# Kernel optimization log

Hardware: AMD Instinct MI355X
Metric: run time of the kernel (lower is better)

## Reference

```python
import jax, jax.numpy as jnp
import numpy as np

N_NODES = 50000
D_FEAT = 128
N_EDGES_1 = 800_000
N_EDGES_2 = 2_400_000


def setup_inputs() -> dict:
    key = jax.random.key(0)
    k = jax.random.split(key, 7)
    x = jax.random.normal(k[0], (N_NODES, D_FEAT), dtype=jnp.float32)
    row1 = jax.random.randint(k[1], (N_EDGES_1,), 0, N_NODES, dtype=jnp.int32)
    col1 = jax.random.randint(k[2], (N_EDGES_1,), 0, N_NODES, dtype=jnp.int32)
    vals1 = jax.random.uniform(k[3], (N_EDGES_1,), dtype=jnp.float32)
    row2 = jax.random.randint(k[4], (N_EDGES_2,), 0, N_NODES, dtype=jnp.int32)
    col2 = jax.random.randint(k[5], (N_EDGES_2,), 0, N_NODES, dtype=jnp.int32)
    vals2 = jax.random.uniform(k[6], (N_EDGES_2,), dtype=jnp.float32)
    return {"x": x, "row1": row1, "col1": col1, "vals1": vals1,
            "row2": row2, "col2": col2, "vals2": vals2}


def _spmm(row, col, vals, x, n_nodes):
    # (A @ x)[i] = sum_{e: row[e]==i} vals[e] * x[col[e]]
    msgs = vals[:, None] * x[col]          # [E, d] gathered, weighted messages
    return jax.ops.segment_sum(msgs, row, num_segments=n_nodes)  # [N, d]


def reference(x, row1, col1, vals1, row2, col2, vals2):
    x1 = _spmm(row1, col1, vals1, x, N_NODES)   # 1-hop aggregation
    x2 = _spmm(row2, col2, vals2, x, N_NODES)   # 2-hop aggregation
    return jnp.concatenate([x1, x2], axis=1)    # [N, 2d]
```

## Files before the change

kernel.cpp:

```cpp
#include <hip/hip_runtime.h>


constexpr int D = 128;
constexpr int OUT_STRIDE = 256;
constexpr int NBMAX = 800;
constexpr int BATCH = 8192;
constexpr int LRECS = 3840;

struct KP {
  const float* x;
  const int* row1; const int* col1; const float* vals1;
  const int* row2; const int* col2; const float* vals2;
  float* out;
  int n, e1, e2, nx4, nb, cap1, cap2, t1, ntasks;
  int* gcur;
  unsigned short* xb;
  uint2* seg1;
  uint2* seg2;
};

__device__ __forceinline__ unsigned short f2b(float f) {
  unsigned u = __float_as_uint(f);
  u += 0x7fffu + ((u >> 16) & 1u);
  return (unsigned short)(u >> 16);
}
__device__ __forceinline__ float blo(unsigned u) { return __uint_as_float(u << 16); }
__device__ __forceinline__ float bhi(unsigned u) { return __uint_as_float(u & 0xffff0000u); }

__global__ void zero_k(KP p) {
  for (int j = threadIdx.x; j < 2 * p.nb; j += 256) p.gcur[j] = 0;
}

__launch_bounds__(512, 2)
__global__ void scatter_k(KP p) {
  __shared__ uint2 srecs[BATCH];
  __shared__ int cnts[NBMAX];
  __shared__ int lstart[NBMAX];
  __shared__ int wsum[8];
  const int tid  = threadIdx.x;
  const int lane = tid & 63;
  const int wid  = tid >> 6;
  const int nb   = p.nb;

  const int task  = blockIdx.x;
  const int hop   = (task >= p.t1);
  const int tbase = (hop ? (task - p.t1) : task) * BATCH;
  const int E     = hop ? p.e2 : p.e1;
  const int m     = min(BATCH, E - tbase);
  const int* rowp = hop ? p.row2 : p.row1;
  const int* colp = hop ? p.col2 : p.col1;
  const float* vp = hop ? p.vals2 : p.vals1;
  const int cap   = hop ? p.cap2 : p.cap1;
  uint2* seg      = hop ? p.seg2 : p.seg1;
  int* gc         = p.gcur + (hop ? nb : 0);

  {
    const int per  = (p.nx4 + (int)gridDim.x - 1) / (int)gridDim.x;
    const int jend = min(p.nx4, (task + 1) * per);
    for (int j = task * per + tid; j < jend; j += 512) {
      const float4 v = ((const float4*)p.x)[j];
      ushort4 o; o.x = f2b(v.x); o.y = f2b(v.y); o.z = f2b(v.z); o.w = f2b(v.w);
      ((ushort4*)p.xb)[j] = o;
    }
  }

  for (int b = tid; b < NBMAX; b += 512) cnts[b] = 0;

  int   rowv[16]; int colv[16]; float valv[16];
  #pragma unroll
  for (int k = 0; k < 4; ++k) {
    const int i4 = tid + (k << 9);
    const int e0 = i4 << 2;
    if (e0 + 3 < m) {
      const int4  r = ((const int4*)(rowp + tbase))[i4];
      const int4  c = ((const int4*)(colp + tbase))[i4];
      const float4 v = ((const float4*)(vp + tbase))[i4];
      rowv[k*4+0] = r.x; rowv[k*4+1] = r.y; rowv[k*4+2] = r.z; rowv[k*4+3] = r.w;
      colv[k*4+0] = c.x; colv[k*4+1] = c.y; colv[k*4+2] = c.z; colv[k*4+3] = c.w;
      valv[k*4+0] = v.x; valv[k*4+1] = v.y; valv[k*4+2] = v.z; valv[k*4+3] = v.w;
    } else {
      #pragma unroll
      for (int c2 = 0; c2 < 4; ++c2) {
        const int e = e0 + c2;
        if (e < m) {
          rowv[k*4+c2] = rowp[tbase + e];
          colv[k*4+c2] = colp[tbase + e];
          valv[k*4+c2] = vp[tbase + e];
        } else {
          rowv[k*4+c2] = -1; colv[k*4+c2] = 0; valv[k*4+c2] = 0.f;
        }
      }
    }
  }
  __syncthreads();

  #pragma unroll
  for (int i = 0; i < 16; ++i) {
    const int r = rowv[i];
    if (r >= 0) {
      const int rk = atomicAdd(&cnts[r >> 6], 1);
      rowv[i] = r | (rk << 16);
    }
  }
  __syncthreads();

  int c0 = 0, c1 = 0, s = 0;
  const int b0 = tid * 2;
  if (b0 < NBMAX) {
    c0 = cnts[b0]; c1 = cnts[b0 + 1];
    s = c0 + c1;
  }
  int acc = s;
  #pragma unroll
  for (int d = 1; d < 64; d <<= 1) { int t = __shfl_up(acc, d); if (lane >= d) acc += t; }
  if (lane == 63) wsum[wid] = acc;
  __syncthreads();
  int woff = 0;
  #pragma unroll
  for (int w = 0; w < 8; ++w) if (w < wid) woff += wsum[w];
  if (b0 < NBMAX) {
    const int ex = woff + acc - s;
    lstart[b0]     = ex;
    lstart[b0 + 1] = ex + c0;
  }
  __syncthreads();

  for (int i = tid; i < nb; i += 512) {
    const int b = (i + task * 37) % nb;
    const int c = cnts[b];
    if (c) {
      const int g = atomicAdd(&gc[b], c);
      cnts[b] = g - lstart[b];
    }
  }
  __syncthreads();

  #pragma unroll
  for (int i = 0; i < 16; ++i) {
    const int rv = rowv[i];
    if (rv >= 0) {
      const int r  = rv & 0xFFFF;
      const int rk = rv >> 16;
      const int b  = r >> 6;
      const unsigned meta = (unsigned)colv[i] | ((unsigned)(r & 63) << 16) | ((unsigned)b << 22);
      srecs[lstart[b] + rk] = make_uint2(meta, __float_as_uint(valv[i]));
    }
  }
  __syncthreads();

  for (int t = tid; t < m; t += 512) {
    const uint2 rec = srecs[t];
    const int b = rec.x >> 22;
    const int pos = t + cnts[b];
    if (pos < cap) seg[(size_t)b * cap + pos] = rec;
  }
}

__launch_bounds__(256)
__global__ void sort_gather_k(KP p) {
  __shared__ uint2 lrecs[LRECS];
  __shared__ int rstart[65];
  __shared__ int lcur[64];
  const int tid  = threadIdx.x;
  const int lane = tid & 63;
  const int wid  = tid >> 6;
  const int nb   = p.nb;
  const int hop  = (blockIdx.x < nb) ? 1 : 0;
  const int b    = hop ? blockIdx.x : blockIdx.x - nb;
  const int cap  = hop ? p.cap2 : p.cap1;
  const uint2* seg = (hop ? p.seg2 : p.seg1) + (size_t)b * cap;
  const int cnt  = min(p.gcur[(hop ? nb : 0) + b], cap);
  const uint4* xq = (const uint4*)p.xb;

  if (tid < 64) lcur[tid] = 0;
  __syncthreads();
  for (int t = tid; t < cnt; t += 256)
    atomicAdd(&lcur[(seg[t].x >> 16) & 63u], 1);
  __syncthreads();

  if (tid < 64) {
    const int c = lcur[tid];
    int acc = c;
    #pragma unroll
    for (int d = 1; d < 64; d <<= 1) { int t = __shfl_up(acc, d); if (lane >= d) acc += t; }
    const int ex = acc - c;
    rstart[tid] = ex;
    lcur[tid] = ex;
    if (tid == 63) rstart[64] = acc;
  }
  __syncthreads();

  for (int t = tid; t < cnt; t += 256) {
    const uint2 rec = seg[t];
    const int rl = (int)((rec.x >> 16) & 63u);
    const int pos = atomicAdd(&lcur[rl], 1);
    lrecs[pos] = rec;
  }
  __syncthreads();

  const int g   = lane >> 4;
  const int sub = lane & 15;
  const int rbase = b * 64;

  for (int r = wid; r < 64; r += 4) {
    const int rg = rbase + r;
    if (rg >= p.n) break;
    const int rs = rstart[r];
    const int re = rstart[r + 1];
    float a0 = 0.f, a1 = 0.f, a2 = 0.f, a3 = 0.f;
    float a4 = 0.f, a5 = 0.f, a6 = 0.f, a7 = 0.f;
    if (re > rs) {
      auto LD = [&](int idx, float& v, uint4& xv) {
        const uint2 q = lrecs[idx < re ? idx : re - 1];
        v = (idx < re) ? __uint_as_float(q.y) : 0.f;
        xv = xq[(q.x & 0xffffu) * 16u + (unsigned)sub];
      };
      #define FMA_G(v, xv)                                            \
        a0 = fmaf(v, blo(xv.x), a0); a1 = fmaf(v, bhi(xv.x), a1);     \
        a2 = fmaf(v, blo(xv.y), a2); a3 = fmaf(v, bhi(xv.y), a3);     \
        a4 = fmaf(v, blo(xv.z), a4); a5 = fmaf(v, bhi(xv.z), a5);     \
        a6 = fmaf(v, blo(xv.w), a6); a7 = fmaf(v, bhi(xv.w), a7);

      float v0, v1, v2, v3; uint4 x0, x1, x2, x3;
      const int j0 = rs + g;
      LD(j0, v0, x0); LD(j0 + 4, v1, x1); LD(j0 + 8, v2, x2); LD(j0 + 12, v3, x3);
      const int iters = (re - rs + 15) >> 4;
      for (int it = 1; it < iters; ++it) {
        const int jn = j0 + (it << 4);
        FMA_G(v0, x0); LD(jn,      v0, x0);
        FMA_G(v1, x1); LD(jn + 4,  v1, x1);
        FMA_G(v2, x2); LD(jn + 8,  v2, x2);
        FMA_G(v3, x3); LD(jn + 12, v3, x3);
      }
      FMA_G(v0, x0); FMA_G(v1, x1); FMA_G(v2, x2); FMA_G(v3, x3);
      #undef FMA_G

      a0 += __shfl_xor(a0, 16); a0 += __shfl_xor(a0, 32);
      a1 += __shfl_xor(a1, 16); a1 += __shfl_xor(a1, 32);
      a2 += __shfl_xor(a2, 16); a2 += __shfl_xor(a2, 32);
      a3 += __shfl_xor(a3, 16); a3 += __shfl_xor(a3, 32);
      a4 += __shfl_xor(a4, 16); a4 += __shfl_xor(a4, 32);
      a5 += __shfl_xor(a5, 16); a5 += __shfl_xor(a5, 32);
      a6 += __shfl_xor(a6, 16); a6 += __shfl_xor(a6, 32);
      a7 += __shfl_xor(a7, 16); a7 += __shfl_xor(a7, 32);
    }
    if (g == 0) {
      float* op = p.out + (size_t)rg * OUT_STRIDE + hop * D + sub * 8;
      ((float4*)op)[0] = make_float4(a0, a1, a2, a3);
      ((float4*)op)[1] = make_float4(a4, a5, a6, a7);
    }
  }
}

extern "C" void kernel_launch(void* const* d_in, const int* in_sizes, int n_in,
                              void* d_out, int out_size, void* d_ws, size_t ws_size,
                              hipStream_t stream) {
  KP p;
  p.x     = (const float*)d_in[0];
  p.row1  = (const int*)  d_in[1];
  p.col1  = (const int*)  d_in[2];
  p.vals1 = (const float*)d_in[3];
  p.row2  = (const int*)  d_in[4];
  p.col2  = (const int*)  d_in[5];
  p.vals2 = (const float*)d_in[6];
  p.out   = (float*)d_out;

  p.e1  = in_sizes[1];
  p.e2  = in_sizes[4];
  p.n   = out_size / OUT_STRIDE;
  p.nx4 = in_sizes[0] / 4;
  p.nb  = (p.n + 63) >> 6;
  if (p.nb > NBMAX || p.n > 65535) return;

  {
    const float m1 = (float)p.e1 / p.nb, m2 = (float)p.e2 / p.nb;
    p.cap1 = ((int)(m1 + 10.f * __builtin_sqrtf(m1) + 64.f) + 7) & ~7;
    p.cap2 = ((int)(m2 + 10.f * __builtin_sqrtf(m2) + 64.f) + 7) & ~7;
    if (p.cap1 > LRECS) p.cap1 = LRECS;
    if (p.cap2 > LRECS) p.cap2 = LRECS;
  }
  p.t1     = (p.e1 + BATCH - 1) / BATCH;
  p.ntasks = p.t1 + (p.e2 + BATCH - 1) / BATCH;

  char* w = (char*)d_ws;
  size_t off = 0;
  p.gcur = (int*)w;                       off += (size_t)(2 * p.nb) * 4;
  off = (off + 15) & ~(size_t)15;
  p.xb   = (unsigned short*)(w + off);    off += (size_t)in_sizes[0] * 2;
  off = (off + 15) & ~(size_t)15;
  p.seg1 = (uint2*)(w + off);             off += (size_t)p.nb * p.cap1 * 8;
  p.seg2 = (uint2*)(w + off);             off += (size_t)p.nb * p.cap2 * 8;
  if (ws_size < off) return;

  zero_k       <<<1,        256, 0, stream>>>(p);
  scatter_k    <<<p.ntasks, 512, 0, stream>>>(p);
  sort_gather_k<<<2 * p.nb, 256, 0, stream>>>(p);
}
```

Baseline: 252.7 us.

## Split sort and gather, quarter-feature bf16 layout for cache-local gathers

Stores the bf16 copy of x split into four 32-feature quarters, each laid out contiguously across nodes. The old sort+gather kernel is split into a sort kernel, which writes the row-sorted records back to the segment buffer along with row offsets, and a gather kernel. In the gather kernel each block handles a single feature quarter, so the working set of x it touches is a quarter of the size and should fit better in L2/MALL. The cost is an extra kernel launch, an extra write and read of the sorted records, and re-reading the records once per quarter.

```diff
diff --git a/kernel.cpp b/kernel.cpp
--- a/kernel.cpp
+++ b/kernel.cpp
@@ -12,8 +12,9 @@
   const int* row1; const int* col1; const float* vals1;
   const int* row2; const int* col2; const float* vals2;
   float* out;
-  int n, e1, e2, nx4, nb, cap1, cap2, t1, ntasks;
+  int n, e1, e2, nx4, nb, cap1, cap2, t1, ntasks, gq;
   int* gcur;
+  int* rstart_g;
   unsigned short* xb;
   uint2* seg1;
   uint2* seg2;
@@ -60,7 +61,11 @@
     for (int j = task * per + tid; j < jend; j += 512) {
       const float4 v = ((const float4*)p.x)[j];
       ushort4 o; o.x = f2b(v.x); o.y = f2b(v.y); o.z = f2b(v.z); o.w = f2b(v.w);
-      ((ushort4*)p.xb)[j] = o;
+      const int node = j >> 5;
+      const int f4   = j & 31;
+      const int q    = f4 >> 3;
+      const int k    = f4 & 7;
+      ((ushort4*)p.xb)[((size_t)q * p.n + node) * 8 + k] = o;
     }
   }
 
@@ -106,10 +111,7 @@
 
   int c0 = 0, c1 = 0, s = 0;
   const int b0 = tid * 2;
-  if (b0 < NBMAX) {
-    c0 = cnts[b0]; c1 = cnts[b0 + 1];
-    s = c0 + c1;
-  }
+  if (b0 < NBMAX) { c0 = cnts[b0]; c1 = cnts[b0 + 1]; s = c0 + c1; }
   int acc = s;
   #pragma unroll
   for (int d = 1; d < 64; d <<= 1) { int t = __shfl_up(acc, d); if (lane >= d) acc += t; }
@@ -157,25 +159,28 @@
 }
 
 __launch_bounds__(256)
-__global__ void sort_gather_k(KP p) {
+__global__ void sortseg_k(KP p) {
   __shared__ uint2 lrecs[LRECS];
-  __shared__ int rstart[65];
   __shared__ int lcur[64];
+  __shared__ int rst[65];
   const int tid  = threadIdx.x;
   const int lane = tid & 63;
-  const int wid  = tid >> 6;
   const int nb   = p.nb;
   const int hop  = (blockIdx.x < nb) ? 1 : 0;
   const int b    = hop ? blockIdx.x : blockIdx.x - nb;
   const int cap  = hop ? p.cap2 : p.cap1;
-  const uint2* seg = (hop ? p.seg2 : p.seg1) + (size_t)b * cap;
+  uint2* seg     = (hop ? p.seg2 : p.seg1) + (size_t)b * cap;
   const int cnt  = min(p.gcur[(hop ? nb : 0) + b], cap);
-  const uint4* xq = (const uint4*)p.xb;
-
+  const int pair = (int)blockIdx.x;
+
+  uint2 rr[15];
   if (tid < 64) lcur[tid] = 0;
   __syncthreads();
-  for (int t = tid; t < cnt; t += 256)
-    atomicAdd(&lcur[(seg[t].x >> 16) & 63u], 1);
+  #pragma unroll
+  for (int k = 0; k < 15; ++k) {
+    const int t = tid + (k << 8);
+    if (t < cnt) { rr[k] = seg[t]; atomicAdd(&lcur[(rr[k].x >> 16) & 63u], 1); }
+  }
   __syncthreads();
 
   if (tid < 64) {
@@ -184,71 +189,92 @@
     #pragma unroll
     for (int d = 1; d < 64; d <<= 1) { int t = __shfl_up(acc, d); if (lane >= d) acc += t; }
     const int ex = acc - c;
-    rstart[tid] = ex;
+    rst[tid] = ex;
     lcur[tid] = ex;
-    if (tid == 63) rstart[64] = acc;
-  }
-  __syncthreads();
-
-  for (int t = tid; t < cnt; t += 256) {
-    const uint2 rec = seg[t];
-    const int rl = (int)((rec.x >> 16) & 63u);
-    const int pos = atomicAdd(&lcur[rl], 1);
-    lrecs[pos] = rec;
-  }
-  __syncthreads();
-
-  const int g   = lane >> 4;
-  const int sub = lane & 15;
-  const int rbase = b * 64;
-
-  for (int r = wid; r < 64; r += 4) {
-    const int rg = rbase + r;
-    if (rg >= p.n) break;
-    const int rs = rstart[r];
-    const int re = rstart[r + 1];
-    float a0 = 0.f, a1 = 0.f, a2 = 0.f, a3 = 0.f;
-    float a4 = 0.f, a5 = 0.f, a6 = 0.f, a7 = 0.f;
-    if (re > rs) {
-      auto LD = [&](int idx, float& v, uint4& xv) {
-        const uint2 q = lrecs[idx < re ? idx : re - 1];
-        v = (idx < re) ? __uint_as_float(q.y) : 0.f;
-        xv = xq[(q.x & 0xffffu) * 16u + (unsigned)sub];
-      };
-      #define FMA_G(v, xv)                                            \
-        a0 = fmaf(v, blo(xv.x), a0); a1 = fmaf(v, bhi(xv.x), a1);     \
-        a2 = fmaf(v, blo(xv.y), a2); a3 = fmaf(v, bhi(xv.y), a3);     \
-        a4 = fmaf(v, blo(xv.z), a4); a5 = fmaf(v, bhi(xv.z), a5);     \
-        a6 = fmaf(v, blo(xv.w), a6); a7 = fmaf(v, bhi(xv.w), a7);
-
-      float v0, v1, v2, v3; uint4 x0, x1, x2, x3;
-      const int j0 = rs + g;
-      LD(j0, v0, x0); LD(j0 + 4, v1, x1); LD(j0 + 8, v2, x2); LD(j0 + 12, v3, x3);
-      const int iters = (re - rs + 15) >> 4;
-      for (int it = 1; it < iters; ++it) {
-        const int jn = j0 + (it << 4);
-        FMA_G(v0, x0); LD(jn,      v0, x0);
-        FMA_G(v1, x1); LD(jn + 4,  v1, x1);
-        FMA_G(v2, x2); LD(jn + 8,  v2, x2);
-        FMA_G(v3, x3); LD(jn + 12, v3, x3);
+    if (tid == 63) rst[64] = acc;
+  }
+  __syncthreads();
+
+  #pragma unroll
+  for (int k = 0; k < 15; ++k) {
+    const int t = tid + (k << 8);
+    if (t < cnt) lrecs[atomicAdd(&lcur[(rr[k].x >> 16) & 63u], 1)] = rr[k];
+  }
+  __syncthreads();
+
+  for (int t = tid; t < cnt; t += 256) seg[t] = lrecs[t];
+  if (tid < 65) p.rstart_g[(size_t)pair * 65 + tid] = rst[tid];
+}
+
+__launch_bounds__(256)
+__global__ void gather_k(KP p) {
+  __shared__ uint2 lrecs[LRECS];
+  __shared__ int rst[65];
+  const int tid  = threadIdx.x;
+  const int lane = tid & 63;
+  const int wid  = tid >> 6;
+  const int g    = lane >> 3;
+  const int sub  = lane & 7;
+  const int nb   = p.nb;
+  const int bid  = (int)blockIdx.x;
+  const int q    = (bid & 7) >> 1;
+  const int idx  = ((bid >> 3) << 1) | (bid & 1);
+  const int stride = 2 * p.gq;
+  const int pairs  = 2 * nb;
+  const uint2* xq2 = (const uint2*)(p.xb + (size_t)q * p.n * 32);
+
+  for (int j = idx; j < pairs; j += stride) {
+    const int hop = (j < nb) ? 1 : 0;
+    const int b   = hop ? j : j - nb;
+    const int cap = hop ? p.cap2 : p.cap1;
+    const uint2* seg = (hop ? p.seg2 : p.seg1) + (size_t)b * cap;
+
+    if (tid < 65) rst[tid] = p.rstart_g[(size_t)j * 65 + tid];
+    __syncthreads();
+    const int cnt = rst[64];
+
+    for (int t = tid; t < cnt; t += 256) {
+      const unsigned long long rv =
+        __builtin_nontemporal_load((const unsigned long long*)(seg + t));
+      lrecs[t] = *(const uint2*)&rv;
+    }
+    __syncthreads();
+
+    const int rbase = b * 64;
+    for (int r = wid; r < 64; r += 4) {
+      const int rg = rbase + r;
+      if (rg >= p.n) break;
+      const int rs = rst[r];
+      const int re = rst[r + 1];
+      float a0 = 0.f, a1 = 0.f, a2 = 0.f, a3 = 0.f;
+      if (re > rs) {
+        int i2 = rs + g;
+        uint2 qA = lrecs[i2 < re ? i2 : re - 1];
+        float vA = (i2 < re) ? __uint_as_float(qA.y) : 0.f;
+        uint2 xA = xq2[(size_t)(qA.x & 0xffffu) * 8u + (unsigned)sub];
+        for (int jn = rs + 8; jn < re; jn += 8) {
+          i2 = jn + g;
+          const uint2 qB = lrecs[i2 < re ? i2 : re - 1];
+          const float vB = (i2 < re) ? __uint_as_float(qB.y) : 0.f;
+          const uint2 xB = xq2[(size_t)(qB.x & 0xffffu) * 8u + (unsigned)sub];
+          a0 = fmaf(vA, blo(xA.x), a0); a1 = fmaf(vA, bhi(xA.x), a1);
+          a2 = fmaf(vA, blo(xA.y), a2); a3 = fmaf(vA, bhi(xA.y), a3);
+          vA = vB; xA = xB;
+        }
+        a0 = fmaf(vA, blo(xA.x), a0); a1 = fmaf(vA, bhi(xA.x), a1);
+        a2 = fmaf(vA, blo(xA.y), a2); a3 = fmaf(vA, bhi(xA.y), a3);
+        #pragma unroll
+        for (int d = 8; d < 64; d <<= 1) {
+          a0 += __shfl_xor(a0, d); a1 += __shfl_xor(a1, d);
+          a2 += __shfl_xor(a2, d); a3 += __shfl_xor(a3, d);
+        }
       }
-      FMA_G(v0, x0); FMA_G(v1, x1); FMA_G(v2, x2); FMA_G(v3, x3);
-      #undef FMA_G
-
-      a0 += __shfl_xor(a0, 16); a0 += __shfl_xor(a0, 32);
-      a1 += __shfl_xor(a1, 16); a1 += __shfl_xor(a1, 32);
-      a2 += __shfl_xor(a2, 16); a2 += __shfl_xor(a2, 32);
-      a3 += __shfl_xor(a3, 16); a3 += __shfl_xor(a3, 32);
-      a4 += __shfl_xor(a4, 16); a4 += __shfl_xor(a4, 32);
-      a5 += __shfl_xor(a5, 16); a5 += __shfl_xor(a5, 32);
-      a6 += __shfl_xor(a6, 16); a6 += __shfl_xor(a6, 32);
-      a7 += __shfl_xor(a7, 16); a7 += __shfl_xor(a7, 32);
-    }
-    if (g == 0) {
-      float* op = p.out + (size_t)rg * OUT_STRIDE + hop * D + sub * 8;
-      ((float4*)op)[0] = make_float4(a0, a1, a2, a3);
-      ((float4*)op)[1] = make_float4(a4, a5, a6, a7);
-    }
+      if (g == 0) {
+        float* op = p.out + (size_t)rg * OUT_STRIDE + hop * D + q * 32 + sub * 4;
+        *((float4*)op) = make_float4(a0, a1, a2, a3);
+      }
+    }
+    __syncthreads();
   }
 }
 
@@ -281,6 +307,7 @@
   }
   p.t1     = (p.e1 + BATCH - 1) / BATCH;
   p.ntasks = p.t1 + (p.e2 + BATCH - 1) / BATCH;
+  p.gq     = (2 * p.nb + 7) / 8;
 
   char* w = (char*)d_ws;
   size_t off = 0;
@@ -290,9 +317,12 @@
   off = (off + 15) & ~(size_t)15;
   p.seg1 = (uint2*)(w + off);             off += (size_t)p.nb * p.cap1 * 8;
   p.seg2 = (uint2*)(w + off);             off += (size_t)p.nb * p.cap2 * 8;
+  off = (off + 15) & ~(size_t)15;
+  p.rstart_g = (int*)(w + off);           off += (size_t)(2 * p.nb) * 65 * 4;
   if (ws_size < off) return;
 
-  zero_k       <<<1,        256, 0, stream>>>(p);
-  scatter_k    <<<p.ntasks, 512, 0, stream>>>(p);
-  sort_gather_k<<<2 * p.nb, 256, 0, stream>>>(p);
-}
+  zero_k   <<<1,          256, 0, stream>>>(p);
+  scatter_k<<<p.ntasks,   512, 0, stream>>>(p);
+  sortseg_k<<<2 * p.nb,   256, 0, stream>>>(p);
+  gather_k <<<8 * p.gq,   256, 0, stream>>>(p);
+}
```

Result: slower. 330.1 us (+30.6%).
